# Optimization experiments

Measured on AMD Instinct MI355X. Metric: run time of the kernel, lower is better.

The kernel has to match this reference:

```python
import jax, jax.numpy as jnp
import numpy as np

T, B, NIN, NH = 2048, 16, 1024, 1024
G = 4 * NH  # gate size


def setup_inputs() -> dict:
    key = jax.random.key(0)
    k1, k2, k3, k4 = jax.random.split(key, 4)
    stdv = 1.0 / np.sqrt(NH)
    X = jax.random.normal(k1, (T, B, NIN), dtype=jnp.float32)
    i = jnp.ones((T, B), dtype=jnp.float32)  # all-valid mask
    h0 = jnp.zeros((B, NH), dtype=jnp.float32)
    c0 = jnp.zeros((B, NH), dtype=jnp.float32)
    W_in = jax.random.uniform(k2, (NIN, G), minval=-stdv, maxval=stdv, dtype=jnp.float32)
    W_re = jax.random.uniform(k3, (NH, G), minval=-stdv, maxval=stdv, dtype=jnp.float32)
    b = jax.random.uniform(k4, (G,), minval=-2 * stdv, maxval=2 * stdv, dtype=jnp.float32)
    return {"X": X, "i": i, "h0": h0, "c0": c0, "W_in": W_in, "W_re": W_re, "b": b}


def reference(X, i, h0, c0, W_in, W_re, b):
    # intern = X @ W_in + b, precomputed for all timesteps (big GEMM)
    H = W_re.shape[0]
    intern = jnp.einsum('tbi,ig->tbg', X, W_in) + b  # [T,B,4H]

    def step(carry, inp):
        h, c = carry
        z, m = inp                       # z: [B,4H], m: [B]
        z = z + h @ W_re                 # recurrent contribution
        cell_in = jnp.tanh(z[:, :H])
        in_gate = jax.nn.sigmoid(z[:, H:2 * H])
        fgt_gate = jax.nn.sigmoid(z[:, 2 * H:3 * H])
        out_gate = jax.nn.sigmoid(z[:, 3 * H:])
        c_new = fgt_gate * c + in_gate * cell_in
        y_new = out_gate * jnp.tanh(c_new)
        m = m[:, None]
        c = m * c_new + (1.0 - m) * c    # masked frames keep old cell
        y = m * y_new                    # masked frames output zero
        return (y, c), (y, c)

    (_, d), (Y, C) = jax.lax.scan(step, (h0, c0), (intern, i))
    # Y: [T,B,H] outputs; C: [T,B,H] per-step cell states; d: [B,H] final cell
    return Y, C, d
```

## Files before the change

kernel.cpp:

```cpp
#include <hip/hip_runtime.h>
#include <cstdint>
#include <cstddef>

#define T_STEPS 2048
#define BATCH   16
#define NIN_D   1024
#define NH_D    1024
#define G_D     4096
#define MROWS   32768
#define NWG     64
#define WGT     512
#define HWORDS  (BATCH * NH_D)

typedef short short8 __attribute__((ext_vector_type(8)));
typedef float f32x4  __attribute__((ext_vector_type(4)));
typedef unsigned u32x4 __attribute__((ext_vector_type(4)));
typedef unsigned u32x2 __attribute__((ext_vector_type(2)));

__device__ __forceinline__ unsigned short f2bf(float f) {
  unsigned u = __builtin_bit_cast(unsigned, f);
  u += 0x7FFFu + ((u >> 16) & 1u);
  return (unsigned short)(u >> 16);
}
__device__ __forceinline__ float bf2f(unsigned short h) {
  unsigned u = ((unsigned)h) << 16;
  return __builtin_bit_cast(float, u);
}
__device__ __forceinline__ float sigmoidf_(float x) { return 1.0f / (1.0f + __expf(-x)); }
__device__ __forceinline__ float tanhf_(float x)    { return 2.0f / (1.0f + __expf(-2.0f * x)) - 1.0f; }

__global__ void cast_f32_bf16(const float* __restrict__ in, unsigned short* __restrict__ out, int n4) {
  int idx = blockIdx.x * blockDim.x + threadIdx.x;
  if (idx < n4) {
    float4 v = ((const float4*)in)[idx];
    ushort4 o;
    o.x = f2bf(v.x); o.y = f2bf(v.y); o.z = f2bf(v.z); o.w = f2bf(v.w);
    ((ushort4*)out)[idx] = o;
  }
}

__global__ void transpose_cast(const float* __restrict__ in, unsigned short* __restrict__ out) {
  __shared__ float tile[32][33];
  const int gx = blockIdx.x * 32;
  const int gy = blockIdx.y * 32;
  const int tx = threadIdx.x, ty = threadIdx.y;
  #pragma unroll
  for (int p = 0; p < 4; ++p)
    tile[ty + p * 8][tx] = in[(size_t)(gy + ty + p * 8) * G_D + gx + tx];
  __syncthreads();
  #pragma unroll
  for (int p = 0; p < 4; ++p)
    out[(size_t)(gx + ty + p * 8) * NIN_D + gy + tx] = f2bf(tile[tx][ty + p * 8]);
}

__global__ void init_state(const float* __restrict__ h0, unsigned* __restrict__ hw) {
  int idx = blockIdx.x * blockDim.x + threadIdx.x;
  if (idx < HWORDS) {
    hw[idx] = (unsigned)f2bf(h0[idx]);
    hw[HWORDS + idx] = 0u;
  }
}

__global__ __launch_bounds__(256) void gemm_intern(
    const unsigned short* __restrict__ A,
    const unsigned short* __restrict__ Bt,
    const float* __restrict__ bias,
    unsigned short* __restrict__ Out) {
  __shared__ unsigned short As[128 * 72];
  __shared__ unsigned short Bs[128 * 72];
  const int tid  = threadIdx.x;
  const int lane = tid & 63;
  const int w    = tid >> 6;
  const int r16  = lane & 15;
  const int kgrp = lane >> 4;
  const int wrow = (w >> 1) * 64;
  const int wcol = (w & 1) * 64;
  const int bx = blockIdx.x;
  const int by = blockIdx.y;

  const unsigned short* Ag = A  + (size_t)by * 128 * NIN_D;
  const unsigned short* Bg = Bt + (size_t)bx * 128 * NIN_D;
  const int trow = tid >> 3;
  const int tcol = (tid & 7) * 8;

  f32x4 acc[4][4];
  #pragma unroll
  for (int m = 0; m < 4; ++m)
    #pragma unroll
    for (int n = 0; n < 4; ++n)
      acc[m][n] = (f32x4){0.f, 0.f, 0.f, 0.f};

  for (int kt = 0; kt < 16; ++kt) {
    const int kb = kt * 64;
    __syncthreads();
    #pragma unroll
    for (int p = 0; p < 4; ++p) {
      const int r = trow + p * 32;
      *(uint4*)(&As[r * 72 + tcol]) = *(const uint4*)(Ag + (size_t)r * NIN_D + kb + tcol);
      *(uint4*)(&Bs[r * 72 + tcol]) = *(const uint4*)(Bg + (size_t)r * NIN_D + kb + tcol);
    }
    __syncthreads();
    #pragma unroll
    for (int kk = 0; kk < 2; ++kk) {
      const int ko = kk * 32 + kgrp * 8;
      short8 af[4], bq[4];
      #pragma unroll
      for (int m = 0; m < 4; ++m)
        af[m] = *(const short8*)(&As[(wrow + m * 16 + r16) * 72 + ko]);
      #pragma unroll
      for (int n = 0; n < 4; ++n)
        bq[n] = *(const short8*)(&Bs[(wcol + n * 16 + r16) * 72 + ko]);
      #pragma unroll
      for (int m = 0; m < 4; ++m)
        #pragma unroll
        for (int n = 0; n < 4; ++n)
          acc[m][n] = __builtin_amdgcn_mfma_f32_16x16x32_bf16(af[m], bq[n], acc[m][n], 0, 0, 0);
    }
  }
  #pragma unroll
  for (int n = 0; n < 4; ++n) {
    const int col = bx * 128 + wcol + n * 16 + r16;
    const float bv = bias[col];
    #pragma unroll
    for (int m = 0; m < 4; ++m) {
      const int row0 = by * 128 + wrow + m * 16 + kgrp * 4;
      #pragma unroll
      for (int i = 0; i < 4; ++i)
        Out[(size_t)(row0 + i) * G_D + col] = f2bf(acc[m][n][i] + bv);
    }
  }
}

__device__ __forceinline__ void poll_stage(const unsigned* __restrict__ buf, unsigned tgt,
                                           int tid, unsigned short* __restrict__ h_s) {
  u32x4 q0, q1, q2, q3, q4, q5, q6, q7;
  const unsigned* p0 = buf + (0 * WGT + tid) * 4;
  const unsigned* p1 = buf + (1 * WGT + tid) * 4;
  const unsigned* p2 = buf + (2 * WGT + tid) * 4;
  const unsigned* p3 = buf + (3 * WGT + tid) * 4;
  const unsigned* p4 = buf + (4 * WGT + tid) * 4;
  const unsigned* p5 = buf + (5 * WGT + tid) * 4;
  const unsigned* p6 = buf + (6 * WGT + tid) * 4;
  const unsigned* p7 = buf + (7 * WGT + tid) * 4;
  bool done = false;
  bool first = true;
  do {
    if (!first && !done) __builtin_amdgcn_s_sleep(1);
    first = false;
    if (!done) {
      asm volatile(
          "global_load_dwordx4 %0, %8, off sc0 sc1\n\t"
          "global_load_dwordx4 %1, %9, off sc0 sc1\n\t"
          "global_load_dwordx4 %2, %10, off sc0 sc1\n\t"
          "global_load_dwordx4 %3, %11, off sc0 sc1\n\t"
          "global_load_dwordx4 %4, %12, off sc0 sc1\n\t"
          "global_load_dwordx4 %5, %13, off sc0 sc1\n\t"
          "global_load_dwordx4 %6, %14, off sc0 sc1\n\t"
          "global_load_dwordx4 %7, %15, off sc0 sc1\n\t"
          "s_waitcnt vmcnt(0)"
          : "=v"(q0), "=v"(q1), "=v"(q2), "=v"(q3),
            "=v"(q4), "=v"(q5), "=v"(q6), "=v"(q7)
          : "v"(p0), "v"(p1), "v"(p2), "v"(p3),
            "v"(p4), "v"(p5), "v"(p6), "v"(p7)
          : "memory");
      done = (q0[0] >> 16) == tgt && (q0[1] >> 16) == tgt && (q0[2] >> 16) == tgt && (q0[3] >> 16) == tgt
          && (q1[0] >> 16) == tgt && (q1[1] >> 16) == tgt && (q1[2] >> 16) == tgt && (q1[3] >> 16) == tgt
          && (q2[0] >> 16) == tgt && (q2[1] >> 16) == tgt && (q2[2] >> 16) == tgt && (q2[3] >> 16) == tgt
          && (q3[0] >> 16) == tgt && (q3[1] >> 16) == tgt && (q3[2] >> 16) == tgt && (q3[3] >> 16) == tgt
          && (q4[0] >> 16) == tgt && (q4[1] >> 16) == tgt && (q4[2] >> 16) == tgt && (q4[3] >> 16) == tgt
          && (q5[0] >> 16) == tgt && (q5[1] >> 16) == tgt && (q5[2] >> 16) == tgt && (q5[3] >> 16) == tgt
          && (q6[0] >> 16) == tgt && (q6[1] >> 16) == tgt && (q6[2] >> 16) == tgt && (q6[3] >> 16) == tgt
          && (q7[0] >> 16) == tgt && (q7[1] >> 16) == tgt && (q7[2] >> 16) == tgt && (q7[3] >> 16) == tgt;
    }
  } while (!__all((int)done));
#define STG(i, Q) { \
    const int u_ = 4 * ((i) * WGT + tid); \
    u32x2 o_; \
    o_[0] = (Q[0] & 0xFFFFu) | (Q[1] << 16); \
    o_[1] = (Q[2] & 0xFFFFu) | (Q[3] << 16); \
    *(u32x2*)(h_s + ((u_ >> 10) * 1032 + (u_ & 1023))) = o_; }
  STG(0, q0) STG(1, q1) STG(2, q2) STG(3, q3)
  STG(4, q4) STG(5, q5) STG(6, q6) STG(7, q7)
#undef STG
}

__global__ __launch_bounds__(WGT, 2) void lstm_scan(
    const unsigned short* __restrict__ intern,
    const unsigned short* __restrict__ WreT,
    const float* __restrict__ msk,
    const float* __restrict__ c0,
    unsigned* __restrict__ hw,
    float* __restrict__ Y, float* __restrict__ C, float* __restrict__ D) {
  const int wg = blockIdx.x;
  const int tid = threadIdx.x;
  const int wv = tid >> 6, lane = tid & 63;
  const int r16 = lane & 15, kgrp = lane >> 4;
  const int q = wv & 3, ks = wv >> 2;
  const int j0 = wg * 16;

  __shared__ unsigned short h_s[16 * 1032];
  __shared__ float z_s[8 * 16 * 17];

  short8 wfrag[16];
  {
    const unsigned short* wp = WreT + (size_t)(q * NH_D + j0 + r16) * NH_D + ks * 512 + kgrp * 8;
    #pragma unroll
    for (int kc = 0; kc < 16; ++kc)
      wfrag[kc] = *(const short8*)(wp + kc * 32);
  }

  const int b = tid >> 4, jj = tid & 15;
  const bool gt = tid < 256;
  float creg = 0.f, mreg = 0.f;
  unsigned short ipr[4] = {0, 0, 0, 0};
  if (gt) {
    creg = c0[b * NH_D + j0 + jj];
    mreg = msk[b];
    #pragma unroll
    for (int qq = 0; qq < 4; ++qq)
      ipr[qq] = intern[(size_t)b * G_D + qq * NH_D + j0 + jj];
  }

  poll_stage(hw, 0u, tid, h_s);
  __syncthreads();

  for (int t = 0; t < T_STEPS; ++t) {
    f32x4 acc4[4];
    #pragma unroll
    for (int p = 0; p < 4; ++p) acc4[p] = (f32x4){0.f, 0.f, 0.f, 0.f};
    const int hbase = r16 * 1032 + ks * 512 + kgrp * 8;
    #pragma unroll
    for (int kc = 0; kc < 16; ++kc) {
      short8 a = *(const short8*)(&h_s[hbase + kc * 32]);
      acc4[kc & 3] = __builtin_amdgcn_mfma_f32_16x16x32_bf16(a, wfrag[kc], acc4[kc & 3], 0, 0, 0);
    }
    f32x4 acc = (acc4[0] + acc4[1]) + (acc4[2] + acc4[3]);

    #pragma unroll
    for (int i = 0; i < 4; ++i)
      z_s[((wv)*16 + kgrp * 4 + i) * 17 + r16] = acc[i];
    __syncthreads();

    if (gt) {
      float zq[4];
      #pragma unroll
      for (int qq = 0; qq < 4; ++qq)
        zq[qq] = z_s[((qq)*16 + b) * 17 + jj] + z_s[((4 + qq) * 16 + b) * 17 + jj] + bf2f(ipr[qq]);
      const float cell = tanhf_(zq[0]);
      const float ig = sigmoidf_(zq[1]);
      const float fg = sigmoidf_(zq[2]);
      const float og = sigmoidf_(zq[3]);
      const float cn = fg * creg + ig * cell;
      const float yn = og * tanhf_(cn);
      const float cnew = mreg * cn + (1.0f - mreg) * creg;
      const float ynew = mreg * yn;
      creg = cnew;

      if (t < T_STEPS - 1) {
        unsigned* dst = hw + (size_t)((t + 1) & 1) * HWORDS;
        __hip_atomic_store(&dst[b * NH_D + j0 + jj],
                           (((unsigned)(t + 1)) << 16) | (unsigned)f2bf(ynew),
                           __ATOMIC_RELAXED, __HIP_MEMORY_SCOPE_AGENT);
      }

      const size_t ob = ((size_t)t * BATCH + b) * NH_D + j0 + jj;
      __builtin_nontemporal_store(ynew, &Y[ob]);
      __builtin_nontemporal_store(cnew, &C[ob]);
      if (t < T_STEPS - 1) {
        const unsigned short* ipn = intern + ((size_t)(t + 1) * BATCH + b) * G_D;
        #pragma unroll
        for (int qq = 0; qq < 4; ++qq)
          ipr[qq] = ipn[qq * NH_D + j0 + jj];
        mreg = msk[(t + 1) * BATCH + b];
      }
    }

    if (t < T_STEPS - 1)
      poll_stage(hw + (size_t)((t + 1) & 1) * HWORDS, (unsigned)(t + 1), tid, h_s);
    __syncthreads();
  }
  if (gt) D[b * NH_D + j0 + jj] = creg;
}

extern "C" void kernel_launch(void* const* d_in, const int* in_sizes, int n_in,
                              void* d_out, int out_size, void* d_ws, size_t ws_size,
                              hipStream_t stream) {
  const float* X     = (const float*)d_in[0];
  const float* imask = (const float*)d_in[1];
  const float* h0    = (const float*)d_in[2];
  const float* c0    = (const float*)d_in[3];
  const float* Win   = (const float*)d_in[4];
  const float* Wre   = (const float*)d_in[5];
  const float* bias  = (const float*)d_in[6];
  float* out = (float*)d_out;

  char* ws = (char*)d_ws;
  unsigned short* Xbf    = (unsigned short*)(ws);
  unsigned short* WinT   = (unsigned short*)(ws + 67108864);
  unsigned short* WreT   = (unsigned short*)(ws + 75497472);
  unsigned short* intern = (unsigned short*)(ws + 83886080);
  unsigned*       hw     = (unsigned*)(ws);

  float* Y = out;
  float* C = out + (size_t)T_STEPS * BATCH * NH_D;
  float* D = out + (size_t)2 * T_STEPS * BATCH * NH_D;

  {
    int n4 = (MROWS * NIN_D) / 4;
    cast_f32_bf16<<<dim3((n4 + 255) / 256), dim3(256), 0, stream>>>(X, Xbf, n4);
  }
  transpose_cast<<<dim3(G_D / 32, NIN_D / 32), dim3(32, 8), 0, stream>>>(Win, WinT);
  transpose_cast<<<dim3(G_D / 32, NH_D / 32),  dim3(32, 8), 0, stream>>>(Wre, WreT);

  gemm_intern<<<dim3(G_D / 128, MROWS / 128), dim3(256), 0, stream>>>(Xbf, WinT, bias, intern);

  init_state<<<dim3(64), dim3(256), 0, stream>>>(h0, hw);

  lstm_scan<<<dim3(NWG), dim3(WGT), 0, stream>>>(intern, WreT, imask, c0, hw, Y, C, D);
}
```

Measured before the change: 7.622 ms.

## Replace tagged-word polling with packed bf16 payload plus per-wave sentinel flags

Cross-workgroup hidden-state exchange changes in two ways. Before, each bf16 value travelled in its own 32-bit word with a step tag and consumers repeatedly polled the whole 64KB buffer. Now two bf16 values are packed per word, so the payload halves, and readiness is signalled by one flag per producing wave. Consumers spin only on the 512 small flags, then read the payload once. This is meant to cut polling traffic and contention, but it adds an extra round trip (flag, then payload) and a full vmcnt wait that also waits on the Y/C output stores before signalling.

```diff
diff --git a/kernel.cpp b/kernel.cpp
--- a/kernel.cpp
+++ b/kernel.cpp
@@ -10,12 +10,12 @@
 #define MROWS   32768
 #define NWG     64
 #define WGT     512
-#define HWORDS  (BATCH * NH_D)
+#define PWORDS  8192
+#define SENTN   512
 
 typedef short short8 __attribute__((ext_vector_type(8)));
 typedef float f32x4  __attribute__((ext_vector_type(4)));
 typedef unsigned u32x4 __attribute__((ext_vector_type(4)));
-typedef unsigned u32x2 __attribute__((ext_vector_type(2)));
 
 __device__ __forceinline__ unsigned short f2bf(float f) {
   unsigned u = __builtin_bit_cast(unsigned, f);
@@ -53,12 +53,14 @@
     out[(size_t)(gx + ty + p * 8) * NIN_D + gy + tx] = f2bf(tile[tx][ty + p * 8]);
 }
 
-__global__ void init_state(const float* __restrict__ h0, unsigned* __restrict__ hw) {
+__global__ void init_state(const float* __restrict__ h0, unsigned* __restrict__ pay,
+                           unsigned* __restrict__ sent) {
   int idx = blockIdx.x * blockDim.x + threadIdx.x;
-  if (idx < HWORDS) {
-    hw[idx] = (unsigned)f2bf(h0[idx]);
-    hw[HWORDS + idx] = 0u;
-  }
+  if (idx < PWORDS) {
+    unsigned lo = f2bf(h0[2 * idx]), hi = f2bf(h0[2 * idx + 1]);
+    pay[idx] = lo | (hi << 16);
+  }
+  if (idx < 2 * SENTN) sent[idx] = 0u;
 }
 
 __global__ __launch_bounds__(256) void gemm_intern(
@@ -131,56 +133,25 @@
   }
 }
 
-__device__ __forceinline__ void poll_stage(const unsigned* __restrict__ buf, unsigned tgt,
-                                           int tid, unsigned short* __restrict__ h_s) {
-  u32x4 q0, q1, q2, q3, q4, q5, q6, q7;
+__device__ __forceinline__ void sweep_stage(const unsigned* __restrict__ buf, int tid,
+                                            unsigned short* __restrict__ h_s) {
+  u32x4 a0, a1, a2, a3;
   const unsigned* p0 = buf + (0 * WGT + tid) * 4;
   const unsigned* p1 = buf + (1 * WGT + tid) * 4;
   const unsigned* p2 = buf + (2 * WGT + tid) * 4;
   const unsigned* p3 = buf + (3 * WGT + tid) * 4;
-  const unsigned* p4 = buf + (4 * WGT + tid) * 4;
-  const unsigned* p5 = buf + (5 * WGT + tid) * 4;
-  const unsigned* p6 = buf + (6 * WGT + tid) * 4;
-  const unsigned* p7 = buf + (7 * WGT + tid) * 4;
-  bool done = false;
-  bool first = true;
-  do {
-    if (!first && !done) __builtin_amdgcn_s_sleep(1);
-    first = false;
-    if (!done) {
-      asm volatile(
-          "global_load_dwordx4 %0, %8, off sc0 sc1\n\t"
-          "global_load_dwordx4 %1, %9, off sc0 sc1\n\t"
-          "global_load_dwordx4 %2, %10, off sc0 sc1\n\t"
-          "global_load_dwordx4 %3, %11, off sc0 sc1\n\t"
-          "global_load_dwordx4 %4, %12, off sc0 sc1\n\t"
-          "global_load_dwordx4 %5, %13, off sc0 sc1\n\t"
-          "global_load_dwordx4 %6, %14, off sc0 sc1\n\t"
-          "global_load_dwordx4 %7, %15, off sc0 sc1\n\t"
-          "s_waitcnt vmcnt(0)"
-          : "=v"(q0), "=v"(q1), "=v"(q2), "=v"(q3),
-            "=v"(q4), "=v"(q5), "=v"(q6), "=v"(q7)
-          : "v"(p0), "v"(p1), "v"(p2), "v"(p3),
-            "v"(p4), "v"(p5), "v"(p6), "v"(p7)
-          : "memory");
-      done = (q0[0] >> 16) == tgt && (q0[1] >> 16) == tgt && (q0[2] >> 16) == tgt && (q0[3] >> 16) == tgt
-          && (q1[0] >> 16) == tgt && (q1[1] >> 16) == tgt && (q1[2] >> 16) == tgt && (q1[3] >> 16) == tgt
-          && (q2[0] >> 16) == tgt && (q2[1] >> 16) == tgt && (q2[2] >> 16) == tgt && (q2[3] >> 16) == tgt
-          && (q3[0] >> 16) == tgt && (q3[1] >> 16) == tgt && (q3[2] >> 16) == tgt && (q3[3] >> 16) == tgt
-          && (q4[0] >> 16) == tgt && (q4[1] >> 16) == tgt && (q4[2] >> 16) == tgt && (q4[3] >> 16) == tgt
-          && (q5[0] >> 16) == tgt && (q5[1] >> 16) == tgt && (q5[2] >> 16) == tgt && (q5[3] >> 16) == tgt
-          && (q6[0] >> 16) == tgt && (q6[1] >> 16) == tgt && (q6[2] >> 16) == tgt && (q6[3] >> 16) == tgt
-          && (q7[0] >> 16) == tgt && (q7[1] >> 16) == tgt && (q7[2] >> 16) == tgt && (q7[3] >> 16) == tgt;
-    }
-  } while (!__all((int)done));
-#define STG(i, Q) { \
-    const int u_ = 4 * ((i) * WGT + tid); \
-    u32x2 o_; \
-    o_[0] = (Q[0] & 0xFFFFu) | (Q[1] << 16); \
-    o_[1] = (Q[2] & 0xFFFFu) | (Q[3] << 16); \
-    *(u32x2*)(h_s + ((u_ >> 10) * 1032 + (u_ & 1023))) = o_; }
-  STG(0, q0) STG(1, q1) STG(2, q2) STG(3, q3)
-  STG(4, q4) STG(5, q5) STG(6, q6) STG(7, q7)
+  asm volatile(
+      "global_load_dwordx4 %0, %4, off sc0 sc1\n\t"
+      "global_load_dwordx4 %1, %5, off sc0 sc1\n\t"
+      "global_load_dwordx4 %2, %6, off sc0 sc1\n\t"
+      "global_load_dwordx4 %3, %7, off sc0 sc1\n\t"
+      "s_waitcnt vmcnt(0)"
+      : "=v"(a0), "=v"(a1), "=v"(a2), "=v"(a3)
+      : "v"(p0), "v"(p1), "v"(p2), "v"(p3)
+      : "memory");
+#define STG(i, A) { const int Qi = (i) * WGT + tid; \
+    *(u32x4*)((char*)h_s + (Qi >> 7) * 2064 + (Qi & 127) * 16) = A; }
+  STG(0, a0) STG(1, a1) STG(2, a2) STG(3, a3)
 #undef STG
 }
 
@@ -189,7 +160,8 @@
     const unsigned short* __restrict__ WreT,
     const float* __restrict__ msk,
     const float* __restrict__ c0,
-    unsigned* __restrict__ hw,
+    unsigned* __restrict__ pay,
+    unsigned* __restrict__ sent,
     float* __restrict__ Y, float* __restrict__ C, float* __restrict__ D) {
   const int wg = blockIdx.x;
   const int tid = threadIdx.x;
@@ -198,7 +170,7 @@
   const int q = wv & 3, ks = wv >> 2;
   const int j0 = wg * 16;
 
-  __shared__ unsigned short h_s[16 * 1032];
+  __shared__ __attribute__((aligned(16))) unsigned short h_s[16 * 1032];
   __shared__ float z_s[8 * 16 * 17];
 
   short8 wfrag[16];
@@ -221,7 +193,7 @@
       ipr[qq] = intern[(size_t)b * G_D + qq * NH_D + j0 + jj];
   }
 
-  poll_stage(hw, 0u, tid, h_s);
+  sweep_stage(pay, tid, h_s);
   __syncthreads();
 
   for (int t = 0; t < T_STEPS; ++t) {
@@ -238,7 +210,7 @@
 
     #pragma unroll
     for (int i = 0; i < 4; ++i)
-      z_s[((wv)*16 + kgrp * 4 + i) * 17 + r16] = acc[i];
+      z_s[(wv * 16 + kgrp * 4 + i) * 17 + r16] = acc[i];
     __syncthreads();
 
     if (gt) {
@@ -257,26 +229,42 @@
       creg = cnew;
 
       if (t < T_STEPS - 1) {
-        unsigned* dst = hw + (size_t)((t + 1) & 1) * HWORDS;
-        __hip_atomic_store(&dst[b * NH_D + j0 + jj],
-                           (((unsigned)(t + 1)) << 16) | (unsigned)f2bf(ynew),
-                           __ATOMIC_RELAXED, __HIP_MEMORY_SCOPE_AGENT);
+        const unsigned short yb = f2bf(ynew);
+        const unsigned prt = (unsigned)(unsigned short)__shfl_xor((int)(unsigned)yb, 1);
+        if ((tid & 1) == 0) {
+          unsigned* dst = pay + (size_t)((t + 1) & 1) * PWORDS;
+          __hip_atomic_store(&dst[b * 512 + ((j0 + jj) >> 1)],
+                             ((unsigned)yb) | (prt << 16),
+                             __ATOMIC_RELAXED, __HIP_MEMORY_SCOPE_AGENT);
+        }
       }
-
       const size_t ob = ((size_t)t * BATCH + b) * NH_D + j0 + jj;
       __builtin_nontemporal_store(ynew, &Y[ob]);
       __builtin_nontemporal_store(cnew, &C[ob]);
-      if (t < T_STEPS - 1) {
+    }
+
+    if (t < T_STEPS - 1) {
+      asm volatile("s_waitcnt vmcnt(0)" ::: "memory");
+      if (lane == 0)
+        __hip_atomic_store(&sent[(size_t)((t + 1) & 1) * SENTN + wg * 8 + wv],
+                           (unsigned)(t + 1), __ATOMIC_RELAXED, __HIP_MEMORY_SCOPE_AGENT);
+
+      if (gt) {
         const unsigned short* ipn = intern + ((size_t)(t + 1) * BATCH + b) * G_D;
         #pragma unroll
         for (int qq = 0; qq < 4; ++qq)
           ipr[qq] = ipn[qq * NH_D + j0 + jj];
         mreg = msk[(t + 1) * BATCH + b];
       }
-    }
-
-    if (t < T_STEPS - 1)
-      poll_stage(hw + (size_t)((t + 1) & 1) * HWORDS, (unsigned)(t + 1), tid, h_s);
+
+      const unsigned* sp = sent + (size_t)((t + 1) & 1) * SENTN + tid;
+      const unsigned tgt = (unsigned)(t + 1);
+      while (__hip_atomic_load(sp, __ATOMIC_RELAXED, __HIP_MEMORY_SCOPE_AGENT) < tgt)
+        __builtin_amdgcn_s_sleep(1);
+      __syncthreads();
+
+      sweep_stage(pay + (size_t)((t + 1) & 1) * PWORDS, tid, h_s);
+    }
     __syncthreads();
   }
   if (gt) D[b * NH_D + j0 + jj] = creg;
@@ -299,7 +287,8 @@
   unsigned short* WinT   = (unsigned short*)(ws + 67108864);
   unsigned short* WreT   = (unsigned short*)(ws + 75497472);
   unsigned short* intern = (unsigned short*)(ws + 83886080);
-  unsigned*       hw     = (unsigned*)(ws);
+  unsigned*       pay    = (unsigned*)(ws);
+  unsigned*       sent   = (unsigned*)(ws + 65536);
 
   float* Y = out;
   float* C = out + (size_t)T_STEPS * BATCH * NH_D;
@@ -314,7 +303,7 @@
 
   gemm_intern<<<dim3(G_D / 128, MROWS / 128), dim3(256), 0, stream>>>(Xbf, WinT, bias, intern);
 
-  init_state<<<dim3(64), dim3(256), 0, stream>>>(h0, hw);
-
-  lstm_scan<<<dim3(NWG), dim3(WGT), 0, stream>>>(intern, WreT, imask, c0, hw, Y, C, D);
-}
+  init_state<<<dim3(32), dim3(256), 0, stream>>>(h0, pay, sent);
+
+  lstm_scan<<<dim3(NWG), dim3(WGT), 0, stream>>>(intern, WreT, imask, c0, pay, sent, Y, C, D);
+}
```

After: 10.19 ms. 1.34x slower.
